# Kernel tuning notes

Hardware: AMD Instinct MI355X
Metric: run time of the kernel (lower is better)

Reference implementation:

```python
import jax, jax.numpy as jnp
import numpy as np

B, S, E = 2, 2048, 5120
HQ, HKV, HD = 32, 8, 128          # q heads, kv heads, head_dim (hard-coded 128 in source)
DQ, DKV = HQ * HD, HKV * HD       # 4096, 1024
ROPE_THETA = 1.0e9
NEG = -1e30


def setup_inputs() -> dict:
    key = jax.random.key(0)
    k0, k1, k2, k3, k4 = jax.random.split(key, 5)
    x = jax.random.normal(k0, (B, S, E), jnp.float32)
    wq = jax.random.normal(k1, (DQ, E), jnp.float32) * 0.02
    wk = jax.random.normal(k2, (DKV, E), jnp.float32) * 0.02
    wv = jax.random.normal(k3, (DKV, E), jnp.float32) * 0.02
    wo = jax.random.normal(k4, (E, DQ), jnp.float32) * 0.02
    # rotary frequencies: complex freqs_cis[s, HD//2] = exp(i * s * theta^{-2j/HD})
    inv_freq = 1.0 / (ROPE_THETA ** (jnp.arange(0, HD, 2, dtype=jnp.float32) / HD))  # [64]
    ang = jnp.arange(S, dtype=jnp.float32)[:, None] * inv_freq[None, :]              # [S, 64]
    return {
        "x": x,
        "freqs_cos": jnp.cos(ang),
        "freqs_sin": jnp.sin(ang),
        "wq": wq, "wk": wk, "wv": wv, "wo": wo,
    }


def _apply_rope(t, cos, sin):
    # t: [b, s, h, HD//2, 2] viewed as complex pairs; cos/sin: [1, s, 1, HD//2]
    tr, ti = t[..., 0], t[..., 1]
    out = jnp.stack([tr * cos - ti * sin, tr * sin + ti * cos], axis=-1)
    b, s, h = t.shape[0], t.shape[1], t.shape[2]
    return out.reshape(b, s, h, HD)


def reference(x, freqs_cos, freqs_sin, wq, wk, wv, wo):
    b, s, _ = x.shape
    q = (x @ wq.T).reshape(b, s, HQ, HD // 2, 2)
    k = (x @ wk.T).reshape(b, s, HKV, HD // 2, 2)
    v = (x @ wv.T).reshape(b, s, HKV, HD)
    cos = freqs_cos[:s][None, :, None, :]
    sin = freqs_sin[:s][None, :, None, :]
    q = _apply_rope(q, cos, sin)                       # [b, s, HQ, HD]
    k = _apply_rope(k, cos, sin)                       # [b, s, HKV, HD]
    # GQA repeat_kv (repeat_interleave along head dim)
    k = jnp.repeat(k, HQ // HKV, axis=2)               # [b, s, HQ, HD]
    v = jnp.repeat(v, HQ // HKV, axis=2)
    q = q.transpose(0, 2, 1, 3)                        # [b, HQ, s, HD]
    k = k.transpose(0, 2, 1, 3)
    v = v.transpose(0, 2, 1, 3)
    scale = 1.0 / np.sqrt(HD).astype(np.float32)
    scores = jnp.einsum('bhqd,bhkd->bhqk', q, k) * scale
    causal = jnp.tril(jnp.ones((s, s), dtype=bool))
    scores = jnp.where(causal[None, None], scores, NEG)
    attn = jax.nn.softmax(scores, axis=-1)
    out = jnp.einsum('bhqk,bhkd->bhqd', attn, v)       # [b, HQ, s, HD]
    out = out.transpose(0, 2, 1, 3).reshape(b, s, DQ)
    return out @ wo.T                                  # [b, s, E]
```

## Files before the change

kernel.cpp:

```cpp
#include <hip/hip_runtime.h>


typedef unsigned short u16;
typedef __bf16 bf16x8 __attribute__((ext_vector_type(8)));
typedef __bf16 bf16x4 __attribute__((ext_vector_type(4)));
typedef float f32x4 __attribute__((ext_vector_type(4)));

__device__ __forceinline__ u16 f2bf(float f) {
  unsigned u = __builtin_bit_cast(unsigned, f);
  u += 0x7fff + ((u >> 16) & 1);
  return (u16)(u >> 16);
}
__device__ __forceinline__ float bf2f(u16 h) {
  unsigned u = ((unsigned)h) << 16;
  return __builtin_bit_cast(float, u);
}

__device__ __forceinline__ float exp2_hw(float x) {
#if __has_builtin(__builtin_amdgcn_exp2f)
  return __builtin_amdgcn_exp2f(x);
#else
  return __expf(x * 0.6931471805599453f);
#endif
}

__device__ __forceinline__ void gload_lds16(const u16* g, u16* lds) {
  __builtin_amdgcn_global_load_lds(
      (const __attribute__((address_space(1))) void*)g,
      (__attribute__((address_space(3))) void*)lds, 16, 0, 0);
}

__device__ __forceinline__ f32x4 mfma16(bf16x8 a, bf16x8 b, f32x4 c) {
  return __builtin_amdgcn_mfma_f32_16x16x32_bf16(a, b, c, 0, 0, 0);
}

#define VMW(N) asm volatile("s_waitcnt vmcnt(" #N ")" ::: "memory")
#define BAR()  __builtin_amdgcn_s_barrier()
#define SCB()  __builtin_amdgcn_sched_barrier(0)

__global__ __launch_bounds__(256) void cvt_kernel(const float4* __restrict__ in,
                                                  uint2* __restrict__ out, int n4) {
  int i = blockIdx.x * blockDim.x + threadIdx.x;
  if (i >= n4) return;
  float4 v = in[i];
  unsigned lo = (unsigned)f2bf(v.x) | ((unsigned)f2bf(v.y) << 16);
  unsigned hi = (unsigned)f2bf(v.z) | ((unsigned)f2bf(v.w) << 16);
  out[i] = make_uint2(lo, hi);
}

__global__ __launch_bounds__(256) void rope_kernel(u16* __restrict__ t,
                                                   const float* __restrict__ fcos,
                                                   const float* __restrict__ fsin,
                                                   int hsh, float scale, int total) {
  int idx = blockIdx.x * blockDim.x + threadIdx.x;
  if (idx >= total) return;
  int j = idx & 63;
  int s = (idx >> (6 + hsh)) & 2047;
  float c = fcos[s * 64 + j], sn = fsin[s * 64 + j];
  unsigned* p = (unsigned*)(t + (size_t)idx * 2);
  unsigned v = *p;
  float tr = bf2f((u16)(v & 0xffffu)), ti = bf2f((u16)(v >> 16));
  float orr = (tr * c - ti * sn) * scale;
  float oi  = (tr * sn + ti * c) * scale;
  *p = (unsigned)f2bf(orr) | ((unsigned)f2bf(oi) << 16);
}

template <int MODE>
__global__ __launch_bounds__(256) void gemm_bt(const u16* __restrict__ A,
                                               const u16* __restrict__ B,
                                               void* __restrict__ Cout,
                                               int M, int N, int K) {
  __shared__ u16 As[8192];
  __shared__ u16 Bs[8192];
  const int tid = threadIdx.x;
  const int lane = tid & 63, wave = tid >> 6;
  const int wm = wave >> 1, wn = wave & 1;
  int gx = gridDim.x, nwg = gx * gridDim.y;
  int lin = blockIdx.y * gx + blockIdx.x;
  if ((nwg & 7) == 0) lin = (lin & 7) * (nwg >> 3) + (lin >> 3);
  const int m0 = (lin / gx) * 128, n0 = (lin % gx) * 128;
  const int lc = lane & 15, lg = lane >> 4;

  f32x4 acc[4][4] = {};
  const int sr = tid >> 3, sc = tid & 7;

  for (int kt = 0; kt < K; kt += 64) {
    __syncthreads();
#pragma unroll
    for (int q = 0; q < 4; ++q) {
      int r = q * 32 + sr;
      int cc = sc ^ (r & 7);
      gload_lds16(A + (size_t)(m0 + r) * K + kt + cc * 8, &As[q * 2048 + tid * 8]);
      gload_lds16(B + (size_t)(n0 + r) * K + kt + cc * 8, &Bs[q * 2048 + tid * 8]);
    }
    __syncthreads();
#pragma unroll
    for (int ks = 0; ks < 2; ++ks) {
      bf16x8 af[4], bfr[4];
#pragma unroll
      for (int m = 0; m < 4; ++m) {
        int r = wm * 64 + m * 16 + lc;
        int gc = ks * 4 + lg;
        af[m] = *(const bf16x8*)&As[r * 64 + ((gc ^ (r & 7)) * 8)];
      }
#pragma unroll
      for (int n = 0; n < 4; ++n) {
        int r = wn * 64 + n * 16 + lc;
        int gc = ks * 4 + lg;
        bfr[n] = *(const bf16x8*)&Bs[r * 64 + ((gc ^ (r & 7)) * 8)];
      }
#pragma unroll
      for (int m = 0; m < 4; ++m)
#pragma unroll
        for (int n = 0; n < 4; ++n)
          acc[m][n] = mfma16(af[m], bfr[n], acc[m][n]);
    }
  }

#pragma unroll
  for (int m = 0; m < 4; ++m) {
#pragma unroll
    for (int n = 0; n < 4; ++n) {
#pragma unroll
      for (int i = 0; i < 4; ++i) {
        int gm = m0 + wm * 64 + m * 16 + lg * 4 + i;
        int gn = n0 + wn * 64 + n * 16 + lc;
        float v = acc[m][n][i];
        if (MODE == 0) {
          ((u16*)Cout)[(size_t)gm * N + gn] = f2bf(v);
        } else {
          size_t addr = ((size_t)((gm >> 11) * 8 + (gn >> 7)) * 128 + (gn & 127)) * 2048 +
                        (gm & 2047);
          ((u16*)Cout)[addr] = f2bf(v);
        }
      }
    }
  }
}

template <int OUT_F32>
__global__ __launch_bounds__(512, 2) void gemm256(const u16* __restrict__ A,
                                                  const u16* __restrict__ B,
                                                  void* __restrict__ Cout,
                                                  int M, int N, int K) {
  __shared__ u16 lds[2][2][2][8192];
  const int tid = threadIdx.x, lane = tid & 63, wave = tid >> 6;
  const int wm = wave >> 2;
  const int wn = wave & 3;
  const int lc = lane & 15, lg = lane >> 4;
  const int srow = lane >> 3;
  const int cc8  = ((lane & 7) ^ srow) * 8;
  const int bh   = wn >> 1;
  const int sb   = wm * 2 + (wn & 1);

  int gx = gridDim.x, nwg = gx * gridDim.y;
  int lin = blockIdx.y * gx + blockIdx.x;
  if ((nwg & 7) == 0) lin = (lin & 7) * (nwg >> 3) + (lin >> 3);
  const int m0 = (lin / gx) * 256, n0 = (lin % gx) * 256;

  auto stA = [&](int buf, int kcol, int rowBase) {
    int rb = rowBase + wn * 8;
    gload_lds16(A + (size_t)(m0 + wm * 128 + rb + srow) * K + kcol + cc8,
                &lds[buf][0][wm][rb * 64 + lane * 8]);
  };
  auto stB = [&](int buf, int kcol, int rowBase) {
    int rb = rowBase + sb * 8;
    gload_lds16(B + (size_t)(n0 + bh * 128 + rb + srow) * K + kcol + cc8,
                &lds[buf][1][bh][rb * 64 + lane * 8]);
  };

  f32x4 acc[8][4] = {};
  bf16x8 af[4][2], bfv[4][2];

  stA(0, 0, 0);  stB(0, 0, 0);
  stA(0, 0, 32); stB(0, 0, 64);
  stB(0, 0, 32); stB(0, 0, 96);
  stA(0, 0, 64); stA(0, 0, 96);
  VMW(4);
  BAR();

  const int nk = K >> 6;
  for (int t = 0; t < nk; ++t) {
    const int cur = t & 1, nxt = cur ^ 1;
    const int kn = (t + 1) << 6;
    const bool hasNext = (t + 1 < nk);
    const u16* Ah = &lds[cur][0][wm][0];
    const u16* Bh = &lds[cur][1][bh][0];

    if (hasNext) { stA(nxt, kn, 0); stB(nxt, kn, 0); }
#pragma unroll
    for (int m = 0; m < 4; ++m)
#pragma unroll
      for (int kg = 0; kg < 2; ++kg) {
        int r = m * 16 + lc;
        af[m][kg] = *(const bf16x8*)&Ah[r * 64 + (((kg * 4 + lg) ^ (r & 7)) * 8)];
      }
#pragma unroll
    for (int n = 0; n < 2; ++n)
#pragma unroll
      for (int kg = 0; kg < 2; ++kg) {
        int r = (wn & 1) * 64 + n * 16 + lc;
        bfv[n][kg] = *(const bf16x8*)&Bh[r * 64 + (((kg * 4 + lg) ^ (r & 7)) * 8)];
      }
    VMW(4);
    BAR(); SCB();
    __builtin_amdgcn_s_setprio(1);
#pragma unroll
    for (int m = 0; m < 4; ++m)
#pragma unroll
      for (int n = 0; n < 2; ++n)
#pragma unroll
        for (int kg = 0; kg < 2; ++kg)
          acc[m][n] = mfma16(af[m][kg], bfv[n][kg], acc[m][n]);
    __builtin_amdgcn_s_setprio(0);
    SCB(); BAR();

    if (hasNext) { stA(nxt, kn, 32); stB(nxt, kn, 64); }
#pragma unroll
    for (int n = 2; n < 4; ++n)
#pragma unroll
      for (int kg = 0; kg < 2; ++kg) {
        int r = (wn & 1) * 64 + n * 16 + lc;
        bfv[n][kg] = *(const bf16x8*)&Bh[r * 64 + (((kg * 4 + lg) ^ (r & 7)) * 8)];
      }
    VMW(4);
    BAR(); SCB();
    __builtin_amdgcn_s_setprio(1);
#pragma unroll
    for (int m = 0; m < 4; ++m)
#pragma unroll
      for (int n = 2; n < 4; ++n)
#pragma unroll
        for (int kg = 0; kg < 2; ++kg)
          acc[m][n] = mfma16(af[m][kg], bfv[n][kg], acc[m][n]);
    __builtin_amdgcn_s_setprio(0);
    SCB(); BAR();

    if (hasNext) { stB(nxt, kn, 32); stB(nxt, kn, 96); }
#pragma unroll
    for (int m = 0; m < 4; ++m)
#pragma unroll
      for (int kg = 0; kg < 2; ++kg) {
        int r = 64 + m * 16 + lc;
        af[m][kg] = *(const bf16x8*)&Ah[r * 64 + (((kg * 4 + lg) ^ (r & 7)) * 8)];
      }
    BAR(); SCB();
    __builtin_amdgcn_s_setprio(1);
#pragma unroll
    for (int m = 0; m < 4; ++m)
#pragma unroll
      for (int n = 0; n < 2; ++n)
#pragma unroll
        for (int kg = 0; kg < 2; ++kg)
          acc[4 + m][n] = mfma16(af[m][kg], bfv[n][kg], acc[4 + m][n]);
    __builtin_amdgcn_s_setprio(0);
    SCB(); BAR();

    if (hasNext) { stA(nxt, kn, 64); stA(nxt, kn, 96); }
    VMW(4);
    BAR(); SCB();
    __builtin_amdgcn_s_setprio(1);
#pragma unroll
    for (int m = 0; m < 4; ++m)
#pragma unroll
      for (int n = 2; n < 4; ++n)
#pragma unroll
        for (int kg = 0; kg < 2; ++kg)
          acc[4 + m][n] = mfma16(af[m][kg], bfv[n][kg], acc[4 + m][n]);
    __builtin_amdgcn_s_setprio(0);
    SCB(); BAR();
  }

#pragma unroll
  for (int m = 0; m < 8; ++m) {
#pragma unroll
    for (int n = 0; n < 4; ++n) {
#pragma unroll
      for (int i = 0; i < 4; ++i) {
        int gm = m0 + wm * 128 + m * 16 + lg * 4 + i;
        int gn = n0 + wn * 64 + n * 16 + lc;
        float v = acc[m][n][i];
        if (OUT_F32) ((float*)Cout)[(size_t)gm * N + gn] = v;
        else         ((u16*)Cout)[(size_t)gm * N + gn] = f2bf(v);
      }
    }
  }
}

__global__ __launch_bounds__(256) void attn_kernel(const u16* __restrict__ Q,
                                                   const u16* __restrict__ Kg,
                                                   const u16* __restrict__ VT,
                                                   u16* __restrict__ AO) {
  __shared__ u16 Ks[2][8192];
  __shared__ u16 Vs[2][8192];
  __shared__ u16 P_lds[4][16 * 72];
  const int tid = threadIdx.x, lane = tid & 63, w = tid >> 6;
  const int qt = (int)gridDim.x - 1 - (int)blockIdx.x;
  const int h = blockIdx.y, b = blockIdx.z;
  const int hkv = h >> 2;
  const int q0 = qt * 64;
  const int lc = lane & 15, lg = lane >> 4;

  bf16x8 qf[4];
  {
    const size_t qrow = ((size_t)(b * 2048 + q0 + w * 16 + lc) * 32 + h) * 128;
#pragma unroll
    for (int ks = 0; ks < 4; ++ks) qf[ks] = *(const bf16x8*)&Q[qrow + ks * 32 + lg * 8];
  }

  f32x4 o[8] = {};
  f32x4 lsum = {0.f, 0.f, 0.f, 0.f};

  const int nsteps = qt + 1;
  const size_t kpanel = ((size_t)b * 2048 * 8 + hkv) * 128;
  const size_t vpanel = ((size_t)(b * 8 + hkv) * 128) * 2048;

  auto stage = [&](int buf, int step) {
    const int kv0 = step * 64;
#pragma unroll
    for (int p = 0; p < 4; ++p) {
      int r = p * 16 + (tid >> 4);
      int cc = (tid & 15) ^ (r & 15);
      gload_lds16(Kg + kpanel + (size_t)(kv0 + r) * 1024 + cc * 8,
                  &Ks[buf][p * 2048 + tid * 8]);
    }
#pragma unroll
    for (int p = 0; p < 4; ++p) {
      int r = p * 32 + (tid >> 3);
      int cc = (tid & 7) ^ (r & 7);
      gload_lds16(VT + vpanel + (size_t)r * 2048 + kv0 + cc * 8,
                  &Vs[buf][p * 2048 + tid * 8]);
    }
  };

  stage(0, 0);

  for (int step = 0; step < nsteps; ++step) {
    const int kv0 = step * 64;
    __syncthreads();
    if (step + 1 < nsteps) stage((step + 1) & 1, step + 1);
    const u16* kb = Ks[step & 1];
    const u16* vb = Vs[step & 1];

    f32x4 s[4];
#pragma unroll
    for (int nf = 0; nf < 4; ++nf) s[nf] = f32x4{0.f, 0.f, 0.f, 0.f};
    __builtin_amdgcn_s_setprio(1);
#pragma unroll
    for (int ks = 0; ks < 4; ++ks) {
#pragma unroll
      for (int nf = 0; nf < 4; ++nf) {
        int r = nf * 16 + lc;
        int gc = ks * 4 + lg;
        bf16x8 kf = *(const bf16x8*)&kb[r * 128 + ((gc ^ (r & 15)) * 8)];
        s[nf] = mfma16(kf, qf[ks], s[nf]);
      }
    }
    __builtin_amdgcn_s_setprio(0);

    if (step == qt) {
      int q = q0 + w * 16 + lc;
#pragma unroll
      for (int nf = 0; nf < 4; ++nf) {
#pragma unroll
        for (int i = 0; i < 4; ++i) {
          int kv = kv0 + nf * 16 + lg * 4 + i;
          if (kv > q) s[nf][i] = -1e30f;
        }
      }
    }

#pragma unroll
    for (int nf = 0; nf < 4; ++nf) {
#pragma unroll
      for (int i = 0; i < 4; ++i) s[nf][i] = exp2_hw(s[nf][i]);
      lsum += s[nf];
      bf16x4 pw = {(__bf16)s[nf][0], (__bf16)s[nf][1], (__bf16)s[nf][2], (__bf16)s[nf][3]};
      *(bf16x4*)&P_lds[w][lc * 72 + nf * 16 + lg * 4] = pw;
    }
    asm volatile("s_waitcnt lgkmcnt(0)" ::: "memory");
    __builtin_amdgcn_sched_barrier(0);

    bf16x8 pa[2];
#pragma unroll
    for (int ksv = 0; ksv < 2; ++ksv)
      pa[ksv] = *(const bf16x8*)&P_lds[w][lc * 72 + ksv * 32 + lg * 8];

    __builtin_amdgcn_s_setprio(1);
#pragma unroll
    for (int nfd = 0; nfd < 8; ++nfd) {
#pragma unroll
      for (int ksv = 0; ksv < 2; ++ksv) {
        int r = nfd * 16 + lc;
        int gc = ksv * 4 + lg;
        bf16x8 vf = *(const bf16x8*)&vb[r * 64 + ((gc ^ (r & 7)) * 8)];
        o[nfd] = mfma16(pa[ksv], vf, o[nfd]);
      }
    }
    __builtin_amdgcn_s_setprio(0);
  }

  float t = lsum[0] + lsum[1] + lsum[2] + lsum[3];
  t += __shfl_xor(t, 16, 64);
  t += __shfl_xor(t, 32, 64);
  float linv[4];
#pragma unroll
  for (int i = 0; i < 4; ++i) linv[i] = 1.0f / __shfl(t, lg * 4 + i, 64);

#pragma unroll
  for (int nfd = 0; nfd < 8; ++nfd)
#pragma unroll
    for (int i = 0; i < 4; ++i) {
      int row = q0 + w * 16 + lg * 4 + i;
      AO[((size_t)(b * 2048 + row) * 32 + h) * 128 + nfd * 16 + lc] =
          f2bf(o[nfd][i] * linv[i]);
    }
}

extern "C" void kernel_launch(void* const* d_in, const int* in_sizes, int n_in,
                              void* d_out, int out_size, void* d_ws, size_t ws_size,
                              hipStream_t stream) {
  const float* x    = (const float*)d_in[0];
  const float* fcos = (const float*)d_in[1];
  const float* fsin = (const float*)d_in[2];
  const float* wq   = (const float*)d_in[3];
  const float* wk   = (const float*)d_in[4];
  const float* wv   = (const float*)d_in[5];
  const float* wo   = (const float*)d_in[6];
  float* out = (float*)d_out;

  char* ws = (char*)d_ws;
  u16* xb  = (u16*)(ws + 0);
  u16* wqb = (u16*)(ws + 41943040ull);
  u16* wkb = (u16*)(ws + 83886080ull);
  u16* wvb = (u16*)(ws + 94371840ull);
  u16* Qb  = (u16*)(ws + 104857600ull);
  u16* Kb  = (u16*)(ws + 138412032ull);
  u16* VTb = (u16*)(ws + 146800640ull);
  u16* AOb = xb;
  u16* wob = wqb;

  auto cvt = [&](const float* src, u16* dst, int nelem) {
    int n4 = nelem / 4;
    cvt_kernel<<<dim3((n4 + 255) / 256), dim3(256), 0, stream>>>((const float4*)src,
                                                                 (uint2*)dst, n4);
  };
  cvt(x, xb, 2 * 2048 * 5120);
  cvt(wq, wqb, 4096 * 5120);
  cvt(wk, wkb, 1024 * 5120);
  cvt(wv, wvb, 1024 * 5120);

  dim3 blk(256);
  gemm256<0><<<dim3(16, 16), dim3(512), 0, stream>>>(xb, wqb, Qb, 4096, 4096, 5120);
  gemm_bt<0><<<dim3(8, 32), blk, 0, stream>>>(xb, wkb, Kb, 4096, 1024, 5120);
  gemm_bt<2><<<dim3(8, 32), blk, 0, stream>>>(xb, wvb, VTb, 4096, 1024, 5120);

  cvt(wo, wob, 5120 * 4096);

  const float qscale = 0.12751743558818574f;
  rope_kernel<<<dim3(8388608 / 256), blk, 0, stream>>>(Qb, fcos, fsin, 5, qscale, 8388608);
  rope_kernel<<<dim3(2097152 / 256), blk, 0, stream>>>(Kb, fcos, fsin, 3, 1.0f, 2097152);

  attn_kernel<<<dim3(32, 32, 2), blk, 0, stream>>>(Qb, Kb, VTb, AOb);

  gemm256<1><<<dim3(20, 16), dim3(512), 0, stream>>>(AOb, wob, out, 4096, 5120, 4096);
}
```

Before: 836.2 us.

## Simplify GEMM pipeline to whole-tile prefetch with two barriers per k-step

Replaces the fine-grained four-phase interleaving of global-to-LDS loads, fragment reads and MFMA groups with a simpler double-buffer scheme. The whole next k-tile is issued at the top of each iteration, the loop waits for the current tile, and it synchronises once before and once after the compute. This removes several barriers and sched_barriers per iteration, cutting sync overhead. The cost is less explicit control over load and MFMA interleaving and over VMEM issue spacing. Correctness depends on the vmcnt(8) count matching the eight outstanding loads.

```diff
diff --git a/kernel.cpp b/kernel.cpp
--- a/kernel.cpp
+++ b/kernel.cpp
@@ -36,7 +36,6 @@
 
 #define VMW(N) asm volatile("s_waitcnt vmcnt(" #N ")" ::: "memory")
 #define BAR()  __builtin_amdgcn_s_barrier()
-#define SCB()  __builtin_amdgcn_sched_barrier(0)
 
 __global__ __launch_bounds__(256) void cvt_kernel(const float4* __restrict__ in,
                                                   uint2* __restrict__ out, int n4) {
@@ -168,26 +167,31 @@
     gload_lds16(B + (size_t)(n0 + bh * 128 + rb + srow) * K + kcol + cc8,
                 &lds[buf][1][bh][rb * 64 + lane * 8]);
   };
+  auto stageAll = [&](int buf, int kcol) {
+    stA(buf, kcol, 0);  stB(buf, kcol, 0);
+    stA(buf, kcol, 32); stB(buf, kcol, 32);
+    stA(buf, kcol, 64); stB(buf, kcol, 64);
+    stA(buf, kcol, 96); stB(buf, kcol, 96);
+  };
 
   f32x4 acc[8][4] = {};
   bf16x8 af[4][2], bfv[4][2];
 
-  stA(0, 0, 0);  stB(0, 0, 0);
-  stA(0, 0, 32); stB(0, 0, 64);
-  stB(0, 0, 32); stB(0, 0, 96);
-  stA(0, 0, 64); stA(0, 0, 96);
-  VMW(4);
-  BAR();
+  stageAll(0, 0);
 
   const int nk = K >> 6;
   for (int t = 0; t < nk; ++t) {
-    const int cur = t & 1, nxt = cur ^ 1;
-    const int kn = (t + 1) << 6;
-    const bool hasNext = (t + 1 < nk);
+    const int cur = t & 1;
+    if (t + 1 < nk) {
+      stageAll(cur ^ 1, (t + 1) << 6);
+      VMW(8);
+    } else {
+      VMW(0);
+    }
+    BAR();
     const u16* Ah = &lds[cur][0][wm][0];
     const u16* Bh = &lds[cur][1][bh][0];
 
-    if (hasNext) { stA(nxt, kn, 0); stB(nxt, kn, 0); }
 #pragma unroll
     for (int m = 0; m < 4; ++m)
 #pragma unroll
@@ -202,8 +206,6 @@
         int r = (wn & 1) * 64 + n * 16 + lc;
         bfv[n][kg] = *(const bf16x8*)&Bh[r * 64 + (((kg * 4 + lg) ^ (r & 7)) * 8)];
       }
-    VMW(4);
-    BAR(); SCB();
     __builtin_amdgcn_s_setprio(1);
 #pragma unroll
     for (int m = 0; m < 4; ++m)
@@ -213,9 +215,7 @@
         for (int kg = 0; kg < 2; ++kg)
           acc[m][n] = mfma16(af[m][kg], bfv[n][kg], acc[m][n]);
     __builtin_amdgcn_s_setprio(0);
-    SCB(); BAR();
-
-    if (hasNext) { stA(nxt, kn, 32); stB(nxt, kn, 64); }
+
 #pragma unroll
     for (int n = 2; n < 4; ++n)
 #pragma unroll
@@ -223,8 +223,6 @@
         int r = (wn & 1) * 64 + n * 16 + lc;
         bfv[n][kg] = *(const bf16x8*)&Bh[r * 64 + (((kg * 4 + lg) ^ (r & 7)) * 8)];
       }
-    VMW(4);
-    BAR(); SCB();
     __builtin_amdgcn_s_setprio(1);
 #pragma unroll
     for (int m = 0; m < 4; ++m)
@@ -234,9 +232,7 @@
         for (int kg = 0; kg < 2; ++kg)
           acc[m][n] = mfma16(af[m][kg], bfv[n][kg], acc[m][n]);
     __builtin_amdgcn_s_setprio(0);
-    SCB(); BAR();
-
-    if (hasNext) { stB(nxt, kn, 32); stB(nxt, kn, 96); }
+
 #pragma unroll
     for (int m = 0; m < 4; ++m)
 #pragma unroll
@@ -244,31 +240,17 @@
         int r = 64 + m * 16 + lc;
         af[m][kg] = *(const bf16x8*)&Ah[r * 64 + (((kg * 4 + lg) ^ (r & 7)) * 8)];
       }
-    BAR(); SCB();
     __builtin_amdgcn_s_setprio(1);
 #pragma unroll
     for (int m = 0; m < 4; ++m)
 #pragma unroll
-      for (int n = 0; n < 2; ++n)
+      for (int n = 0; n < 4; ++n)
 #pragma unroll
         for (int kg = 0; kg < 2; ++kg)
           acc[4 + m][n] = mfma16(af[m][kg], bfv[n][kg], acc[4 + m][n]);
     __builtin_amdgcn_s_setprio(0);
-    SCB(); BAR();
-
-    if (hasNext) { stA(nxt, kn, 64); stA(nxt, kn, 96); }
-    VMW(4);
-    BAR(); SCB();
-    __builtin_amdgcn_s_setprio(1);
-#pragma unroll
-    for (int m = 0; m < 4; ++m)
-#pragma unroll
-      for (int n = 2; n < 4; ++n)
-#pragma unroll
-        for (int kg = 0; kg < 2; ++kg)
-          acc[4 + m][n] = mfma16(af[m][kg], bfv[n][kg], acc[4 + m][n]);
-    __builtin_amdgcn_s_setprio(0);
-    SCB(); BAR();
+
+    BAR();
   }
 
 #pragma unroll
```

New measurement: 854.2 us. 2.2% more time.
